# Optimization experiments

Hardware: AMD Instinct MI355X
Metric: run time of the kernel (lower is better)

The kernel has to match this reference:

```python
import jax, jax.numpy as jnp
import numpy as np

D = 1024
H = 16
DH = D // H
MAX_TYPES = 256
B, L = 8, 1024
EPS = 1e-5


def setup_inputs() -> dict:
    key = jax.random.key(0)
    ks = jax.random.split(key, 16)
    s = 0.02
    return {
        'type_ids': jax.random.randint(ks[0], (B, L), 0, MAX_TYPES),
        'values': jax.random.normal(ks[1], (B, L, 1), jnp.float32),
        'deltas': jax.random.uniform(ks[2], (B, L, 1), jnp.float32),
        'type_emb': jax.random.normal(ks[3], (MAX_TYPES, D), jnp.float32) * s,
        'Wv': jax.random.normal(ks[4], (D, 1), jnp.float32) * s,
        'bv': jnp.zeros((D,), jnp.float32),
        'Wt': jax.random.normal(ks[5], (D, 1), jnp.float32) * s,
        'bt': jnp.zeros((D,), jnp.float32),
        'Win': jax.random.normal(ks[6], (3 * D, D), jnp.float32) * s,
        'bin': jnp.zeros((3 * D,), jnp.float32),
        'Wout': jax.random.normal(ks[7], (D, D), jnp.float32) * s,
        'bout': jnp.zeros((D,), jnp.float32),
        'W1': jax.random.normal(ks[8], (D, D), jnp.float32) * s,
        'b1': jnp.zeros((D,), jnp.float32),
        'W2': jax.random.normal(ks[9], (D, D), jnp.float32) * s,
        'b2': jnp.zeros((D,), jnp.float32),
        'gamma': jnp.ones((D,), jnp.float32),
        'beta': jnp.zeros((D,), jnp.float32),
    }


def _ln(x, gamma, beta):
    mu = jnp.mean(x, axis=-1, keepdims=True)
    var = jnp.mean(jnp.square(x - mu), axis=-1, keepdims=True)
    return (x - mu) * jax.lax.rsqrt(var + EPS) * gamma + beta


def reference(type_ids, values, deltas, type_emb, Wv, bv, Wt, bt,
              Win, bin, Wout, bout, W1, b1, W2, b2, gamma, beta):
    # fused embedding: type lookup + value/time linear projections
    h = type_emb[type_ids] + values @ Wv.T + bv + deltas @ Wt.T + bt  # [B,L,D]
    b, l, d = h.shape
    # multi-head self-attention (explicit weights path, need_weights=True)
    qkv = h @ Win.T + bin  # [B,L,3D]
    q, k, v = jnp.split(qkv, 3, axis=-1)
    q = q.reshape(b, l, H, DH)
    k = k.reshape(b, l, H, DH)
    v = v.reshape(b, l, H, DH)
    scale = 1.0 / jnp.sqrt(jnp.asarray(DH, h.dtype))
    scores = jnp.einsum('blhd,bmhd->bhlm', q, k) * scale  # [B,H,L,L]
    w = jax.nn.softmax(scores, axis=-1)
    attn = jnp.einsum('bhlm,bmhd->blhd', w, v).reshape(b, l, d)
    attn_out = attn @ Wout.T + bout
    h2 = _ln(h + attn_out, gamma, beta)
    ff = jax.nn.relu(h2 @ W1.T + b1) @ W2.T + b2
    h3 = _ln(h2 + ff, gamma, beta)
    pooled = h3.mean(axis=1)  # [B,D]
    attn_tokens = w.mean(axis=1).mean(axis=2)  # mean over heads, then keys -> [B,L]
    return pooled, attn_tokens
```

## Files before the change

### kernel.cpp

```cpp
#include <hip/hip_runtime.h>
#include <hip/hip_bf16.h>


#define Dm 1024
#define Hh 16
#define Bb 8
#define Ll 1024
#define Mm 8192
#define LNEPS 1e-5f

typedef __attribute__((ext_vector_type(8))) short s16x8;
typedef __attribute__((ext_vector_type(4))) short s16x4;
typedef __attribute__((ext_vector_type(4))) float f32x4;
typedef __attribute__((ext_vector_type(16))) float f32x16;

using bf16 = __hip_bfloat16;

__device__ __forceinline__ short f2bs(float f) {
  return __builtin_bit_cast(short, __float2bfloat16(f));
}
__device__ __forceinline__ float b2f(short s) {
  return __builtin_bit_cast(float, ((unsigned)(unsigned short)s) << 16);
}

__device__ __forceinline__ unsigned cvtpk(float lo, float hi) {
  unsigned r;
  asm("v_cvt_pk_bf16_f32 %0, %1, %2" : "=v"(r) : "v"(lo), "v"(hi));
  return r;
}
__device__ __forceinline__ void perm32(unsigned &a, unsigned &b) {
  asm volatile("v_permlane32_swap_b32 %0, %1" : "+v"(a), "+v"(b));
}

__device__ __forceinline__ void gload16(const void* g, void* l) {
  __builtin_amdgcn_global_load_lds(
      (__attribute__((address_space(1))) void*)g,
      (__attribute__((address_space(3))) void*)l, 16, 0, 0);
}

__global__ __launch_bounds__(256) void k_f2b4(
    const float* __restrict__ w0, const float* __restrict__ w1,
    const float* __restrict__ w2, const float* __restrict__ w3,
    bf16* __restrict__ o0, bf16* __restrict__ o1,
    bf16* __restrict__ o2, bf16* __restrict__ o3)
{
  const int bId = blockIdx.x;
  const float* src; bf16* dst; int rel;
  if (bId < 3072)      { src = w0; dst = o0; rel = bId; }
  else if (bId < 4096) { src = w1; dst = o1; rel = bId - 3072; }
  else if (bId < 5120) { src = w2; dst = o2; rel = bId - 4096; }
  else                 { src = w3; dst = o3; rel = bId - 5120; }
  const size_t i = ((size_t)rel * 256 + threadIdx.x) * 4;
  const float4 v = *(const float4*)&src[i];
  s16x4 o;
  o[0] = f2bs(v.x); o[1] = f2bs(v.y); o[2] = f2bs(v.z); o[3] = f2bs(v.w);
  *(s16x4*)&dst[i] = o;
}

__global__ __launch_bounds__(256) void k_embed(
    const int* __restrict__ tids, const float* __restrict__ vals, const float* __restrict__ dels,
    const float* __restrict__ temb, const float* __restrict__ Wv, const float* __restrict__ bv,
    const float* __restrict__ Wt, const float* __restrict__ bt,
    bf16* __restrict__ hb)
{
  const int row = blockIdx.x;
  const int ty = tids[row];
  const float v = vals[row], dl = dels[row];
  const int d0 = threadIdx.x * 4;
  const float4 e  = *(const float4*)&temb[(size_t)ty * Dm + d0];
  const float4 wv = *(const float4*)&Wv[d0];
  const float4 c1 = *(const float4*)&bv[d0];
  const float4 wt = *(const float4*)&Wt[d0];
  const float4 c2 = *(const float4*)&bt[d0];
  s16x4 o;
  o[0] = f2bs(e.x + v * wv.x + c1.x + dl * wt.x + c2.x);
  o[1] = f2bs(e.y + v * wv.y + c1.y + dl * wt.y + c2.y);
  o[2] = f2bs(e.z + v * wv.z + c1.z + dl * wt.z + c2.z);
  o[3] = f2bs(e.w + v * wv.w + c1.w + dl * wt.w + c2.w);
  *(s16x4*)((short*)hb + (size_t)row * Dm + d0) = o;
}

template<bool RELU, bool RES>
__global__ __launch_bounds__(512) void k_gemm8(
    const bf16* __restrict__ A, const bf16* __restrict__ Bt,
    const float* __restrict__ bias, const bf16* __restrict__ res,
    bf16* __restrict__ outB, const int N, const int K)
{
  __shared__ __attribute__((aligned(16))) short lds[49152];
  const int tid = threadIdx.x, lane = tid & 63, wave = tid >> 6;
  const int wr = wave >> 2, wc = wave & 3;
  const int l15 = lane & 15, lg = (lane >> 4) & 3;
  const int bm = blockIdx.x, bn = blockIdx.y;
  const int NT = K >> 6;

  const int rl = tid >> 3;
  const int swz = ((tid & 7) ^ (rl & 7)) * 8;
  const bf16* aSrc = A  + (size_t)(bm * 128 + rl) * K + swz;
  const bf16* bSrc = Bt + (size_t)(bn * 256 + rl) * K + swz;

  f32x4 acc[4][4] = {};

  auto stageA = [&](int t, int h) {
    gload16(aSrc + (size_t)h * 64 * K + t * 64,
            &lds[(t & 1) * 24576 + h * 4096 + tid * 8]);
  };
  auto stageB = [&](int t, int h) {
    gload16(bSrc + (size_t)h * 128 * K + t * 64,
            &lds[(t & 1) * 24576 + 8192 + h * 8192 + tid * 8]);
    gload16(bSrc + (size_t)(h * 128 + 64) * K + t * 64,
            &lds[(t & 1) * 24576 + 8192 + h * 8192 + 4096 + tid * 8]);
  };

  stageA(0, 0); stageA(0, 1); stageB(0, 0); stageB(0, 1);
  if (NT > 1) { stageA(1, 0); stageA(1, 1); }
  asm volatile("s_waitcnt vmcnt(2)" ::: "memory");
  __builtin_amdgcn_sched_barrier(0);
  __builtin_amdgcn_s_barrier();

  for (int t = 0; t < NT; ++t) {
    const int cb = (t & 1) * 24576;
    s16x8 fa[4][2], fb[2][2];

#pragma unroll
    for (int m = 0; m < 4; ++m)
#pragma unroll
      for (int ks = 0; ks < 2; ++ks) {
        const int row = wr * 64 + m * 16 + l15;
        fa[m][ks] = *(const s16x8*)&lds[cb + row * 64 + (((ks * 4 + lg) ^ (row & 7)) << 3)];
      }
#pragma unroll
    for (int n = 0; n < 2; ++n)
#pragma unroll
      for (int ks = 0; ks < 2; ++ks) {
        const int row = wc * 64 + n * 16 + l15;
        fb[n][ks] = *(const s16x8*)&lds[cb + 8192 + row * 64 + (((ks * 4 + lg) ^ (row & 7)) << 3)];
      }
    if (t + 1 < NT) { stageB(t + 1, 0); stageB(t + 1, 1); }
    __builtin_amdgcn_s_barrier();
    asm volatile("s_waitcnt lgkmcnt(0)" ::: "memory");
    __builtin_amdgcn_sched_barrier(0);
    __builtin_amdgcn_s_setprio(1);
#pragma unroll
    for (int m = 0; m < 4; ++m)
#pragma unroll
      for (int n = 0; n < 2; ++n)
#pragma unroll
        for (int ks = 0; ks < 2; ++ks)
          acc[m][n] = __builtin_amdgcn_mfma_f32_16x16x32_bf16(fa[m][ks], fb[n][ks], acc[m][n], 0, 0, 0);
    __builtin_amdgcn_s_setprio(0);
    __builtin_amdgcn_s_barrier();

#pragma unroll
    for (int n = 0; n < 2; ++n)
#pragma unroll
      for (int ks = 0; ks < 2; ++ks) {
        const int row = wc * 64 + (2 + n) * 16 + l15;
        fb[n][ks] = *(const s16x8*)&lds[cb + 8192 + row * 64 + (((ks * 4 + lg) ^ (row & 7)) << 3)];
      }
    if (t + 2 < NT) { stageA(t + 2, 0); stageA(t + 2, 1); }
    __builtin_amdgcn_s_barrier();
    asm volatile("s_waitcnt lgkmcnt(0)" ::: "memory");
    __builtin_amdgcn_sched_barrier(0);
    __builtin_amdgcn_s_setprio(1);
#pragma unroll
    for (int m = 0; m < 4; ++m)
#pragma unroll
      for (int n = 0; n < 2; ++n)
#pragma unroll
        for (int ks = 0; ks < 2; ++ks)
          acc[m][2 + n] = __builtin_amdgcn_mfma_f32_16x16x32_bf16(fa[m][ks], fb[n][ks], acc[m][2 + n], 0, 0, 0);
    __builtin_amdgcn_s_setprio(0);

    if (t + 1 < NT) {
      if (t + 2 < NT) asm volatile("s_waitcnt vmcnt(2)" ::: "memory");
      else            asm volatile("s_waitcnt vmcnt(0)" ::: "memory");
      __builtin_amdgcn_sched_barrier(0);
      __builtin_amdgcn_s_barrier();
    }
  }

#pragma unroll
  for (int n = 0; n < 4; ++n) {
    const int col = bn * 256 + wc * 64 + n * 16 + l15;
    const float bc = bias[col];
#pragma unroll
    for (int m = 0; m < 4; ++m) {
#pragma unroll
      for (int i = 0; i < 4; ++i) {
        const size_t row = (size_t)bm * 128 + wr * 64 + m * 16 + lg * 4 + i;
        float v = acc[m][n][i] + bc;
        if constexpr (RES)  v += b2f(((const short*)res)[row * N + col]);
        if constexpr (RELU) v = fmaxf(v, 0.f);
        outB[row * N + col] = __float2bfloat16(v);
      }
    }
  }
}

__global__ __launch_bounds__(256) void k_vt(const bf16* __restrict__ qkv, bf16* __restrict__ vt)
{
  const int bh = blockIdx.x, lc = blockIdx.y;
  const int b = bh >> 4, h = bh & 15;
  __shared__ short tile[64][72];
  const int r = threadIdx.x >> 2;
  const int c0 = (threadIdx.x & 3) << 4;
  const short* src = (const short*)qkv + ((size_t)(b * Ll + lc * 64 + r)) * 3072 + 2048 + h * 64 + c0;
  const s16x8 x0 = *(const s16x8*)src;
  const s16x8 x1 = *(const s16x8*)(src + 8);
#pragma unroll
  for (int j = 0; j < 8; ++j) { tile[r][c0 + j] = x0[j]; tile[r][c0 + 8 + j] = x1[j]; }
  __syncthreads();
  s16x8 y0, y1;
#pragma unroll
  for (int j = 0; j < 8; ++j) { y0[j] = tile[c0 + j][r]; y1[j] = tile[c0 + 8 + j][r]; }
  short* dst = (short*)vt + ((size_t)(bh * 64 + r)) * Ll + lc * 64 + c0;
  *(s16x8*)dst = y0;
  *(s16x8*)(dst + 8) = y1;
}

__global__ __launch_bounds__(256) void k_attn(
    const bf16* __restrict__ qkv, const bf16* __restrict__ vt, bf16* __restrict__ attnb)
{
  const int bh = blockIdx.x, qb = blockIdx.y;
  const int b = bh >> 4, h = bh & 15;
  __shared__ __attribute__((aligned(16))) short lK[8192];
  __shared__ __attribute__((aligned(16))) short lV[8192];
  const int tid = threadIdx.x, lane = tid & 63, wave = tid >> 6;
  const int l31 = lane & 31, hi = lane >> 5;
  const int r7 = l31 & 7;
  const int qrow = wave * 32;

  s16x8 qf[4];
  {
    const short* qp = (const short*)qkv +
        ((size_t)(b * Ll + qb * 128 + qrow + l31)) * 3072 + h * 64 + hi * 8;
#pragma unroll
    for (int s = 0; s < 4; ++s) qf[s] = *(const s16x8*)(qp + s * 16);
  }

  f32x16 o[2] = {};
  float rsa[4] = {0.f, 0.f, 0.f, 0.f};

  const int sr = tid >> 3;
  const int swz = (tid & 7) ^ (sr & 7);

  auto stage = [&](int mc) {
    const int bo = (mc & 1) * 4096;
    const bf16* gk = qkv + ((size_t)(b * Ll + mc * 64 + sr)) * 3072 + 1024 + h * 64 + swz * 8;
    gload16(gk,                      &lK[bo + tid * 8]);
    gload16(gk + (size_t)32 * 3072,  &lK[bo + 2048 + tid * 8]);
    const bf16* gv = vt + ((size_t)(bh * 64 + sr)) * Ll + mc * 64 + swz * 8;
    gload16(gv,                    &lV[bo + tid * 8]);
    gload16(gv + (size_t)32 * Ll,  &lV[bo + 2048 + tid * 8]);
  };

  stage(0);

  for (int mc = 0; mc < 16; ++mc) {
    asm volatile("s_waitcnt vmcnt(0)" ::: "memory");
    __builtin_amdgcn_s_barrier();
    __builtin_amdgcn_sched_barrier(0);
    if (mc + 1 < 16) stage(mc + 1);
    const int bo = (mc & 1) * 4096;

    f32x16 st[2] = {};
    __builtin_amdgcn_s_setprio(1);
#pragma unroll
    for (int s = 0; s < 4; ++s) {
      const int sl = ((2 * s + hi) ^ r7) << 3;
      const s16x8 kf0 = *(const s16x8*)&lK[bo + l31 * 64 + sl];
      const s16x8 kf1 = *(const s16x8*)&lK[bo + (32 + l31) * 64 + sl];
      st[0] = __builtin_amdgcn_mfma_f32_32x32x16_bf16(kf0, qf[s], st[0], 0, 0, 0);
      st[1] = __builtin_amdgcn_mfma_f32_32x32x16_bf16(kf1, qf[s], st[1], 0, 0, 0);
    }
    __builtin_amdgcn_s_setprio(0);

#pragma unroll
    for (int t = 0; t < 2; ++t) {
#pragma unroll
      for (int r = 0; r < 16; ++r) {
        const float e = exp2f(st[t][r] * 0.18033688f);
        rsa[r & 3] += e;
        st[t][r] = e;
      }
#pragma unroll
      for (int g = 0; g < 2; ++g) {
        unsigned c0 = cvtpk(st[t][8 * g + 0], st[t][8 * g + 1]);
        unsigned c1 = cvtpk(st[t][8 * g + 2], st[t][8 * g + 3]);
        unsigned c2 = cvtpk(st[t][8 * g + 4], st[t][8 * g + 5]);
        unsigned c3 = cvtpk(st[t][8 * g + 6], st[t][8 * g + 7]);
        perm32(c0, c2);
        perm32(c1, c3);
        uint4 wda; wda.x = c0; wda.y = c1; wda.z = c2; wda.w = c3;
        const s16x8 pa = __builtin_bit_cast(s16x8, wda);
        const int s = 2 * t + g;
        const int sl = ((2 * s + hi) ^ r7) << 3;
        const s16x8 vf0 = *(const s16x8*)&lV[bo + l31 * 64 + sl];
        const s16x8 vf1 = *(const s16x8*)&lV[bo + (32 + l31) * 64 + sl];
        o[0] = __builtin_amdgcn_mfma_f32_32x32x16_bf16(pa, vf0, o[0], 0, 0, 0);
        o[1] = __builtin_amdgcn_mfma_f32_32x32x16_bf16(pa, vf1, o[1], 0, 0, 0);
      }
    }
  }

  float rs = (rsa[0] + rsa[1]) + (rsa[2] + rsa[3]);
  rs += __shfl_xor(rs, 32);
  float inv[16];
#pragma unroll
  for (int r = 0; r < 16; ++r)
    inv[r] = 1.f / __shfl(rs, (r & 3) + 8 * (r >> 2) + 4 * hi);
#pragma unroll
  for (int t = 0; t < 2; ++t) {
#pragma unroll
    for (int r = 0; r < 16; ++r) {
      const int q = qb * 128 + qrow + (r & 3) + 8 * (r >> 2) + 4 * hi;
      attnb[((size_t)(b * Ll + q)) * Dm + h * 64 + t * 32 + l31] =
          __float2bfloat16(o[t][r] * inv[r]);
    }
  }
}

__global__ __launch_bounds__(256) void k_ln(const bf16* __restrict__ x,
    const float* __restrict__ gamma, const float* __restrict__ beta,
    bf16* __restrict__ y)
{
  const size_t row = blockIdx.x;
  const int d0 = threadIdx.x * 4;
  const s16x4 xv = *(const s16x4*)((const short*)x + row * Dm + d0);
  float f0 = b2f(xv[0]), f1 = b2f(xv[1]), f2 = b2f(xv[2]), f3 = b2f(xv[3]);
  float s  = (f0 + f1) + (f2 + f3);
  float ss = (f0 * f0 + f1 * f1) + (f2 * f2 + f3 * f3);
#pragma unroll
  for (int m = 1; m < 64; m <<= 1) { s += __shfl_xor(s, m); ss += __shfl_xor(ss, m); }
  __shared__ float red[8];
  const int wv = threadIdx.x >> 6;
  if ((threadIdx.x & 63) == 0) { red[wv] = s; red[4 + wv] = ss; }
  __syncthreads();
  s  = red[0] + red[1] + red[2] + red[3];
  ss = red[4] + red[5] + red[6] + red[7];
  const float mu = s * (1.f / Dm);
  const float rstd = rsqrtf(ss * (1.f / Dm) - mu * mu + LNEPS);
  const float4 g  = *(const float4*)&gamma[d0];
  const float4 be = *(const float4*)&beta[d0];
  s16x4 o;
  o[0] = f2bs((f0 - mu) * rstd * g.x + be.x);
  o[1] = f2bs((f1 - mu) * rstd * g.y + be.y);
  o[2] = f2bs((f2 - mu) * rstd * g.z + be.z);
  o[3] = f2bs((f3 - mu) * rstd * g.w + be.w);
  *(s16x4*)((short*)y + row * Dm + d0) = o;
}

__global__ __launch_bounds__(256) void k_pool_part(const bf16* __restrict__ h3, float* __restrict__ part)
{
  const int b = blockIdx.x, lcn = blockIdx.y, dz = blockIdx.z;
  const int d = dz * 256 + threadIdx.x;
  float s = 0.f;
#pragma unroll 4
  for (int l = 0; l < 64; ++l)
    s += b2f(((const short*)h3)[((size_t)(b * Ll + lcn * 64 + l)) * Dm + d]);
  part[((size_t)(b * 16 + lcn)) * Dm + d] = s;
}

__global__ __launch_bounds__(256) void k_pool_fin(const float* __restrict__ part, float* __restrict__ out)
{
  const int b = blockIdx.x;
  const int d = blockIdx.y * 256 + threadIdx.x;
  float s = 0.f;
#pragma unroll
  for (int c = 0; c < 16; ++c) s += part[((size_t)(b * 16 + c)) * Dm + d];
  out[b * Dm + d] = s * (1.f / Ll);
  out[(size_t)Mm + b * Dm + d] = 1.f / Ll;
}

extern "C" void kernel_launch(void* const* d_in, const int* in_sizes, int n_in,
                              void* d_out, int out_size, void* d_ws, size_t ws_size,
                              hipStream_t stream) {
  const int*   tids  = (const int*)  d_in[0];
  const float* vals  = (const float*)d_in[1];
  const float* dels  = (const float*)d_in[2];
  const float* temb  = (const float*)d_in[3];
  const float* Wv    = (const float*)d_in[4];
  const float* bv    = (const float*)d_in[5];
  const float* Wt    = (const float*)d_in[6];
  const float* bt    = (const float*)d_in[7];
  const float* Win   = (const float*)d_in[8];
  const float* bin   = (const float*)d_in[9];
  const float* Wout  = (const float*)d_in[10];
  const float* bout  = (const float*)d_in[11];
  const float* W1    = (const float*)d_in[12];
  const float* b1    = (const float*)d_in[13];
  const float* W2    = (const float*)d_in[14];
  const float* b2    = (const float*)d_in[15];
  const float* gamma = (const float*)d_in[16];
  const float* beta  = (const float*)d_in[17];
  float* out = (float*)d_out;

  char* w = (char*)d_ws;
  const size_t MB = 1ull << 20;
  bf16*  hb    = (bf16*) (w + 0);
  bf16*  qkv   = (bf16*) (w + 16 * MB);
  bf16*  vtb   = (bf16*) (w + 64 * MB);
  bf16*  attnb = (bf16*) (w + 80 * MB);
  bf16*  x1b   = (bf16*) (w + 16 * MB);
  bf16*  h2b   = (bf16*) (w + 32 * MB);
  bf16*  ff1   = (bf16*) (w + 48 * MB);
  bf16*  x2b   = (bf16*) (w + 64 * MB);
  bf16*  h3b   = (bf16*) (w + 80 * MB);
  bf16*  WinB  = (bf16*) (w + 96 * MB);
  bf16*  WoutB = (bf16*) (w + 102 * MB);
  bf16*  W1B   = (bf16*) (w + 104 * MB);
  bf16*  W2B   = (bf16*) (w + 106 * MB);
  float* part  = (float*)(w + 108 * MB);

  k_f2b4<<<6144, 256, 0, stream>>>(Win, Wout, W1, W2, WinB, WoutB, W1B, W2B);

  k_embed<<<Mm, 256, 0, stream>>>(tids, vals, dels, temb, Wv, bv, Wt, bt, hb);

  k_gemm8<false, false><<<dim3(64, 12), 512, 0, stream>>>(
      hb, WinB, bin, nullptr, qkv, 3072, 1024);

  k_vt<<<dim3(128, 16), 256, 0, stream>>>(qkv, vtb);
  k_attn<<<dim3(128, 8), 256, 0, stream>>>(qkv, vtb, attnb);

  k_gemm8<false, true><<<dim3(64, 4), 512, 0, stream>>>(
      attnb, WoutB, bout, hb, x1b, 1024, 1024);

  k_ln<<<Mm, 256, 0, stream>>>(x1b, gamma, beta, h2b);

  k_gemm8<true, false><<<dim3(64, 4), 512, 0, stream>>>(
      h2b, W1B, b1, nullptr, ff1, 1024, 1024);

  k_gemm8<false, true><<<dim3(64, 4), 512, 0, stream>>>(
      ff1, W2B, b2, h2b, x2b, 1024, 1024);

  k_ln<<<Mm, 256, 0, stream>>>(x2b, gamma, beta, h3b);

  k_pool_part<<<dim3(8, 16, 4), 256, 0, stream>>>(h3b, part);
  k_pool_fin<<<dim3(8, 4), 256, 0, stream>>>(part, out);
}
```

Before: 247.4 us.

## Double query rows per attention wave and fold softmax scale into Q weights

Each attention wave now handles 64 query rows in two groups, so K and V fragments loaded from LDS are reused across both groups. This halves the attention grid to 512 blocks. The softmax scale times log2(e) is folded into the Q slice of Win and its bias during weight conversion and the QKV GEMM epilogue, which removes a multiply per score. The raw hardware exp2 intrinsic replaces exp2f. The cost is more registers (two sets of Q fragments and accumulators), fewer blocks in flight, and rounding to bf16 after scaling Q.

```diff
diff --git a/kernel.cpp b/kernel.cpp
--- a/kernel.cpp
+++ b/kernel.cpp
@@ -8,6 +8,7 @@
 #define Ll 1024
 #define Mm 8192
 #define LNEPS 1e-5f
+#define QSCALE 0.18033688f
 
 typedef __attribute__((ext_vector_type(8))) short s16x8;
 typedef __attribute__((ext_vector_type(4))) short s16x4;
@@ -46,14 +47,15 @@
 {
   const int bId = blockIdx.x;
   const float* src; bf16* dst; int rel;
-  if (bId < 3072)      { src = w0; dst = o0; rel = bId; }
+  float sc = 1.f;
+  if (bId < 3072)      { src = w0; dst = o0; rel = bId; if (bId < 1024) sc = QSCALE; }
   else if (bId < 4096) { src = w1; dst = o1; rel = bId - 3072; }
   else if (bId < 5120) { src = w2; dst = o2; rel = bId - 4096; }
   else                 { src = w3; dst = o3; rel = bId - 5120; }
   const size_t i = ((size_t)rel * 256 + threadIdx.x) * 4;
   const float4 v = *(const float4*)&src[i];
   s16x4 o;
-  o[0] = f2bs(v.x); o[1] = f2bs(v.y); o[2] = f2bs(v.z); o[3] = f2bs(v.w);
+  o[0] = f2bs(v.x * sc); o[1] = f2bs(v.y * sc); o[2] = f2bs(v.z * sc); o[3] = f2bs(v.w * sc);
   *(s16x4*)&dst[i] = o;
 }
 
@@ -80,7 +82,7 @@
   *(s16x4*)((short*)hb + (size_t)row * Dm + d0) = o;
 }
 
-template<bool RELU, bool RES>
+template<bool RELU, bool RES, bool QS>
 __global__ __launch_bounds__(512) void k_gemm8(
     const bf16* __restrict__ A, const bf16* __restrict__ Bt,
     const float* __restrict__ bias, const bf16* __restrict__ res,
@@ -182,7 +184,8 @@
 #pragma unroll
   for (int n = 0; n < 4; ++n) {
     const int col = bn * 256 + wc * 64 + n * 16 + l15;
-    const float bc = bias[col];
+    float bc = bias[col];
+    if constexpr (QS) { if (col < 1024) bc *= QSCALE; }
 #pragma unroll
     for (int m = 0; m < 4; ++m) {
 #pragma unroll
@@ -228,18 +231,19 @@
   const int tid = threadIdx.x, lane = tid & 63, wave = tid >> 6;
   const int l31 = lane & 31, hi = lane >> 5;
   const int r7 = l31 & 7;
-  const int qrow = wave * 32;
-
-  s16x8 qf[4];
-  {
+  const int qbase = qb * 256 + wave * 64;
+
+  s16x8 qf[2][4];
+#pragma unroll
+  for (int g = 0; g < 2; ++g) {
     const short* qp = (const short*)qkv +
-        ((size_t)(b * Ll + qb * 128 + qrow + l31)) * 3072 + h * 64 + hi * 8;
-#pragma unroll
-    for (int s = 0; s < 4; ++s) qf[s] = *(const s16x8*)(qp + s * 16);
+        ((size_t)(b * Ll + qbase + g * 32 + l31)) * 3072 + h * 64 + hi * 8;
+#pragma unroll
+    for (int s = 0; s < 4; ++s) qf[g][s] = *(const s16x8*)(qp + s * 16);
   }
 
-  f32x16 o[2] = {};
-  float rsa[4] = {0.f, 0.f, 0.f, 0.f};
+  f32x16 o[2][2] = {};
+  float rsa[2][4] = {};
 
   const int sr = tid >> 3;
   const int swz = (tid & 7) ^ (sr & 7);
@@ -263,59 +267,71 @@
     if (mc + 1 < 16) stage(mc + 1);
     const int bo = (mc & 1) * 4096;
 
-    f32x16 st[2] = {};
-    __builtin_amdgcn_s_setprio(1);
+    s16x8 kf[4][2], vf[4][2];
 #pragma unroll
     for (int s = 0; s < 4; ++s) {
-      const int sl = ((2 * s + hi) ^ r7) << 3;
-      const s16x8 kf0 = *(const s16x8*)&lK[bo + l31 * 64 + sl];
-      const s16x8 kf1 = *(const s16x8*)&lK[bo + (32 + l31) * 64 + sl];
-      st[0] = __builtin_amdgcn_mfma_f32_32x32x16_bf16(kf0, qf[s], st[0], 0, 0, 0);
-      st[1] = __builtin_amdgcn_mfma_f32_32x32x16_bf16(kf1, qf[s], st[1], 0, 0, 0);
+      const int sl = (((2 * s + hi) ^ r7) << 3);
+      kf[s][0] = *(const s16x8*)&lK[bo + l31 * 64 + sl];
+      kf[s][1] = *(const s16x8*)&lK[bo + (32 + l31) * 64 + sl];
+      vf[s][0] = *(const s16x8*)&lV[bo + l31 * 64 + sl];
+      vf[s][1] = *(const s16x8*)&lV[bo + (32 + l31) * 64 + sl];
     }
-    __builtin_amdgcn_s_setprio(0);
-
-#pragma unroll
-    for (int t = 0; t < 2; ++t) {
+
+#pragma unroll
+    for (int g = 0; g < 2; ++g) {
+      f32x16 st0 = {}, st1 = {};
+      __builtin_amdgcn_s_setprio(1);
+#pragma unroll
+      for (int s = 0; s < 4; ++s) {
+        st0 = __builtin_amdgcn_mfma_f32_32x32x16_bf16(kf[s][0], qf[g][s], st0, 0, 0, 0);
+        st1 = __builtin_amdgcn_mfma_f32_32x32x16_bf16(kf[s][1], qf[g][s], st1, 0, 0, 0);
+      }
+      __builtin_amdgcn_s_setprio(0);
+
 #pragma unroll
       for (int r = 0; r < 16; ++r) {
-        const float e = exp2f(st[t][r] * 0.18033688f);
-        rsa[r & 3] += e;
-        st[t][r] = e;
-      }
-#pragma unroll
-      for (int g = 0; g < 2; ++g) {
-        unsigned c0 = cvtpk(st[t][8 * g + 0], st[t][8 * g + 1]);
-        unsigned c1 = cvtpk(st[t][8 * g + 2], st[t][8 * g + 3]);
-        unsigned c2 = cvtpk(st[t][8 * g + 4], st[t][8 * g + 5]);
-        unsigned c3 = cvtpk(st[t][8 * g + 6], st[t][8 * g + 7]);
+        const float e0 = __builtin_amdgcn_exp2f(st0[r]);
+        const float e1 = __builtin_amdgcn_exp2f(st1[r]);
+        rsa[g][r & 3] += e0 + e1;
+        st0[r] = e0; st1[r] = e1;
+      }
+
+      __builtin_amdgcn_s_setprio(1);
+#pragma unroll
+      for (int ss = 0; ss < 4; ++ss) {
+        const f32x16& src = (ss < 2) ? st0 : st1;
+        const int go = (ss & 1) * 8;
+        unsigned c0 = cvtpk(src[go + 0], src[go + 1]);
+        unsigned c1 = cvtpk(src[go + 2], src[go + 3]);
+        unsigned c2 = cvtpk(src[go + 4], src[go + 5]);
+        unsigned c3 = cvtpk(src[go + 6], src[go + 7]);
         perm32(c0, c2);
         perm32(c1, c3);
         uint4 wda; wda.x = c0; wda.y = c1; wda.z = c2; wda.w = c3;
         const s16x8 pa = __builtin_bit_cast(s16x8, wda);
-        const int s = 2 * t + g;
-        const int sl = ((2 * s + hi) ^ r7) << 3;
-        const s16x8 vf0 = *(const s16x8*)&lV[bo + l31 * 64 + sl];
-        const s16x8 vf1 = *(const s16x8*)&lV[bo + (32 + l31) * 64 + sl];
-        o[0] = __builtin_amdgcn_mfma_f32_32x32x16_bf16(pa, vf0, o[0], 0, 0, 0);
-        o[1] = __builtin_amdgcn_mfma_f32_32x32x16_bf16(pa, vf1, o[1], 0, 0, 0);
-      }
+        o[g][0] = __builtin_amdgcn_mfma_f32_32x32x16_bf16(pa, vf[ss][0], o[g][0], 0, 0, 0);
+        o[g][1] = __builtin_amdgcn_mfma_f32_32x32x16_bf16(pa, vf[ss][1], o[g][1], 0, 0, 0);
+      }
+      __builtin_amdgcn_s_setprio(0);
     }
   }
 
-  float rs = (rsa[0] + rsa[1]) + (rsa[2] + rsa[3]);
-  rs += __shfl_xor(rs, 32);
-  float inv[16];
-#pragma unroll
-  for (int r = 0; r < 16; ++r)
-    inv[r] = 1.f / __shfl(rs, (r & 3) + 8 * (r >> 2) + 4 * hi);
-#pragma unroll
-  for (int t = 0; t < 2; ++t) {
-#pragma unroll
-    for (int r = 0; r < 16; ++r) {
-      const int q = qb * 128 + qrow + (r & 3) + 8 * (r >> 2) + 4 * hi;
-      attnb[((size_t)(b * Ll + q)) * Dm + h * 64 + t * 32 + l31] =
-          __float2bfloat16(o[t][r] * inv[r]);
+#pragma unroll
+  for (int g = 0; g < 2; ++g) {
+    float rs = (rsa[g][0] + rsa[g][1]) + (rsa[g][2] + rsa[g][3]);
+    rs += __shfl_xor(rs, 32);
+    float inv[16];
+#pragma unroll
+    for (int r = 0; r < 16; ++r)
+      inv[r] = 1.f / __shfl(rs, (r & 3) + 8 * (r >> 2) + 4 * hi);
+#pragma unroll
+    for (int t = 0; t < 2; ++t) {
+#pragma unroll
+      for (int r = 0; r < 16; ++r) {
+        const int q = qbase + g * 32 + (r & 3) + 8 * (r >> 2) + 4 * hi;
+        attnb[((size_t)(b * Ll + q)) * Dm + h * 64 + t * 32 + l31] =
+            __float2bfloat16(o[g][t][r] * inv[r]);
+      }
     }
   }
 }
@@ -416,21 +432,21 @@
 
   k_embed<<<Mm, 256, 0, stream>>>(tids, vals, dels, temb, Wv, bv, Wt, bt, hb);
 
-  k_gemm8<false, false><<<dim3(64, 12), 512, 0, stream>>>(
+  k_gemm8<false, false, true><<<dim3(64, 12), 512, 0, stream>>>(
       hb, WinB, bin, nullptr, qkv, 3072, 1024);
 
   k_vt<<<dim3(128, 16), 256, 0, stream>>>(qkv, vtb);
-  k_attn<<<dim3(128, 8), 256, 0, stream>>>(qkv, vtb, attnb);
-
-  k_gemm8<false, true><<<dim3(64, 4), 512, 0, stream>>>(
+  k_attn<<<dim3(128, 4), 256, 0, stream>>>(qkv, vtb, attnb);
+
+  k_gemm8<false, true, false><<<dim3(64, 4), 512, 0, stream>>>(
       attnb, WoutB, bout, hb, x1b, 1024, 1024);
 
   k_ln<<<Mm, 256, 0, stream>>>(x1b, gamma, beta, h2b);
 
-  k_gemm8<true, false><<<dim3(64, 4), 512, 0, stream>>>(
+  k_gemm8<true, false, false><<<dim3(64, 4), 512, 0, stream>>>(
       h2b, W1B, b1, nullptr, ff1, 1024, 1024);
 
-  k_gemm8<false, true><<<dim3(64, 4), 512, 0, stream>>>(
+  k_gemm8<false, true, false><<<dim3(64, 4), 512, 0, stream>>>(
       ff1, W2B, b2, h2b, x2b, 1024, 1024);
 
   k_ln<<<Mm, 256, 0, stream>>>(x2b, gamma, beta, h3b);
```

Measured after the change: 247.1 us. About the same (-0.1%).
